# Kernel tuning notes

Hardware: AMD Instinct MI355X
Metric: run time of the kernel (lower is better)

Reference implementation:

```python
import jax, jax.numpy as jnp
import numpy as np

DIM = 256
D_STATE = 64
D_CONV = 4
EXPAND = 2
D_INNER = EXPAND * DIM          # 512
DT_RANK = DIM // 16             # 16, Mamba default dt_rank='auto'
LN_EPS = 1e-5


def setup_inputs() -> dict:
    key = jax.random.key(0)
    ks = jax.random.split(key, 8)
    B, L = 4, 1024
    s = lambda k, shape, fan: jax.random.normal(k, shape, jnp.float32) / np.sqrt(fan).astype(np.float32)
    inp = {}
    inp['x'] = jax.random.normal(ks[0], (B, L, DIM), jnp.float32)
    inp['C_SA'] = jax.random.normal(ks[1], (B, L, D_STATE), jnp.float32)
    # LayerNorm params
    inp['gamma'] = jnp.ones((DIM,), jnp.float32)
    inp['beta'] = jnp.zeros((DIM,), jnp.float32)
    # Mamba params
    inp['W_in'] = s(ks[2], (2 * D_INNER, DIM), DIM)
    inp['conv_w'] = s(ks[3], (D_INNER, 1, D_CONV), D_CONV)   # depthwise causal conv
    inp['conv_b'] = jnp.zeros((D_INNER,), jnp.float32)
    inp['W_x'] = s(ks[4], (DT_RANK + D_STATE, D_INNER), D_INNER)  # -> (dt_low_rank, B_ssm)
    inp['W_dt'] = s(ks[5], (D_INNER, DT_RANK), DT_RANK)
    # softplus-inverse of 0.01 so initial dt ~ 0.01 (Mamba dt init)
    inp['b_dt'] = jnp.log(jnp.expm1(jnp.full((D_INNER,), 0.01, jnp.float32)))
    # S4D-real init: A = -[1..N]
    inp['A_log'] = jnp.log(jnp.broadcast_to(jnp.arange(1, D_STATE + 1, dtype=jnp.float32), (D_INNER, D_STATE)))
    inp['D'] = jnp.ones((D_INNER,), jnp.float32)
    inp['W_out'] = s(ks[6], (DIM, D_INNER), D_INNER)
    return inp


def reference(x, C_SA, gamma, beta, W_in, conv_w, conv_b, W_x, W_dt, b_dt, A_log, D, W_out):
    B, L, _ = x.shape
    # --- LayerNorm ---
    mu = jnp.mean(x, axis=-1, keepdims=True)
    var = jnp.mean(jnp.square(x - mu), axis=-1, keepdims=True)
    xn = (x - mu) * jax.lax.rsqrt(var + LN_EPS) * gamma + beta
    # --- input projection and gate split ---
    xz = xn @ W_in.T                              # [B,L,2*Di]
    u, z = jnp.split(xz, 2, axis=-1)
    # --- causal depthwise conv1d + SiLU ---
    u_c = jax.lax.conv_general_dilated(
        u.transpose(0, 2, 1), conv_w, (1,), [(D_CONV - 1, 0)],
        feature_group_count=D_INNER,
        dimension_numbers=('NCH', 'OIH', 'NCH'))  # [B,Di,L]
    u = jax.nn.silu(u_c.transpose(0, 2, 1) + conv_b)  # [B,L,Di]
    # --- data-dependent SSM params (C comes from C_SA externally) ---
    dbl = u @ W_x.T                               # [B,L,dt_rank+N]
    dt = jax.nn.softplus(dbl[..., :DT_RANK] @ W_dt.T + b_dt)  # [B,L,Di]
    Bs = dbl[..., DT_RANK:]                       # [B,L,N]
    A = -jnp.exp(A_log)                           # [Di,N]
    # --- selective scan over time ---
    def step(h, t):
        dt_t, B_t, C_t, u_t = t                   # [B,Di],[B,N],[B,N],[B,Di]
        dA = jnp.exp(dt_t[..., None] * A)         # [B,Di,N]
        h = dA * h + (dt_t * u_t)[..., None] * B_t[:, None, :]
        y = jnp.einsum('bdn,bn->bd', h, C_t)
        return h, y
    h0 = jnp.zeros((B, D_INNER, D_STATE), x.dtype)
    xs = (dt.transpose(1, 0, 2), Bs.transpose(1, 0, 2),
          C_SA.transpose(1, 0, 2), u.transpose(1, 0, 2))
    _, ys = jax.lax.scan(step, h0, xs)            # ys: [L,B,Di]
    y = ys.transpose(1, 0, 2) + u * D             # skip connection
    y = y * jax.nn.silu(z)                        # gate
    return y @ W_out.T                            # [B,L,dim]
```

## Files before the change

kernel.cpp:

```cpp
#include <hip/hip_runtime.h>
#include <cstdint>
#include <cstddef>

#define B_    4
#define L_    1024
#define DIM_  256
#define DI_   512
#define NTOK  (B_*L_)
#define NC    32
#define CL    (L_/NC)

__device__ __forceinline__ float siluf_(float x){ return x / (1.0f + __expf(-x)); }
__device__ __forceinline__ float softplusf_(float x){
  return (x > 15.0f) ? x : log1pf(__expf(x));
}

__global__ __launch_bounds__(1024) void k_check(const float* __restrict__ A_log,
    int* __restrict__ flag){
  __shared__ int s_ok;
  int tid = threadIdx.x;
  if (tid == 0) s_ok = 1;
  __syncthreads();
  int ok = 1;
  for (int i = tid; i < 512 * 64; i += 1024){
    int n = i & 63;
    float ref = logf((float)(n + 1));
    float v = A_log[i];
    if (fabsf(v - ref) > 1e-5f * fmaxf(1.0f, fabsf(ref))) ok = 0;
  }
  if (!ok) atomicAnd(&s_ok, 0);
  __syncthreads();
  if (tid == 0) *flag = s_ok;
}

__global__ __launch_bounds__(256) void k_ln_stats(const float* __restrict__ x,
    float* __restrict__ stats){
  int tok  = blockIdx.x * 4 + (threadIdx.x >> 6);
  int lane = threadIdx.x & 63;
  float4 v = *(const float4*)(x + (size_t)tok * DIM_ + lane * 4);
  float s  = v.x + v.y + v.z + v.w;
  float sq = v.x*v.x + v.y*v.y + v.z*v.z + v.w*v.w;
  #pragma unroll
  for (int off = 32; off; off >>= 1){
    s  += __shfl_xor(s,  off, 64);
    sq += __shfl_xor(sq, off, 64);
  }
  if (lane == 0){
    float mu = s * (1.0f / DIM_);
    stats[tok*2]   = mu;
    stats[tok*2+1] = rsqrtf(sq * (1.0f / DIM_) - mu*mu + 1e-5f);
  }
}

__global__ __launch_bounds__(256) void k_gemm1(const float* __restrict__ x,
    const float* __restrict__ stats, const float* __restrict__ gamma,
    const float* __restrict__ beta, const float* __restrict__ Win,
    float* __restrict__ xz){
  __shared__ float As[16][64];
  __shared__ float Bs[16][64];
  int tid = threadIdx.x;
  int mBase = blockIdx.y * 64;
  int nBase = blockIdx.x * 64;
  int tx = tid & 15, ty = tid >> 4;
  int am = tid >> 2, ak = (tid & 3) << 2;
  float mu = stats[(mBase+am)*2], rs = stats[(mBase+am)*2+1];
  float acc[4][4] = {};
  for (int kt = 0; kt < 256; kt += 16){
    float4 av = *(const float4*)(x   + (size_t)(mBase+am)*256 + kt + ak);
    float4 bv = *(const float4*)(Win + (size_t)(nBase+am)*256 + kt + ak);
    float4 gv = *(const float4*)(gamma + kt + ak);
    float4 be = *(const float4*)(beta  + kt + ak);
    As[ak+0][am] = (av.x - mu) * rs * gv.x + be.x;
    As[ak+1][am] = (av.y - mu) * rs * gv.y + be.y;
    As[ak+2][am] = (av.z - mu) * rs * gv.z + be.z;
    As[ak+3][am] = (av.w - mu) * rs * gv.w + be.w;
    Bs[ak+0][am]=bv.x; Bs[ak+1][am]=bv.y; Bs[ak+2][am]=bv.z; Bs[ak+3][am]=bv.w;
    __syncthreads();
    #pragma unroll
    for (int kk = 0; kk < 16; kk++){
      float4 a = *(const float4*)&As[kk][ty*4];
      float4 b = *(const float4*)&Bs[kk][tx*4];
      float ar[4] = {a.x,a.y,a.z,a.w}, br[4] = {b.x,b.y,b.z,b.w};
      #pragma unroll
      for (int i=0;i<4;i++)
        #pragma unroll
        for (int j=0;j<4;j++)
          acc[i][j] += ar[i]*br[j];
    }
    __syncthreads();
  }
  #pragma unroll
  for (int i=0;i<4;i++){
    float4 o = make_float4(acc[i][0],acc[i][1],acc[i][2],acc[i][3]);
    *(float4*)(xz + (size_t)(mBase+ty*4+i)*1024 + nBase + tx*4) = o;
  }
}

__global__ __launch_bounds__(256) void k_conv(const float* __restrict__ xz,
    const float* __restrict__ cw, const float* __restrict__ cb,
    float* __restrict__ uc){
  int g = blockIdx.x * 256 + threadIdx.x;
  int d = g & 511;
  int tok = g >> 9;
  int t = tok & (L_ - 1);
  float w0 = cw[d*4+0], w1 = cw[d*4+1], w2 = cw[d*4+2], w3 = cw[d*4+3];
  const float* up = xz + (size_t)tok * 1024 + d;
  float acc = cb[d] + w3 * up[0];
  if (t >= 1) acc += w2 * up[-1 * 1024];
  if (t >= 2) acc += w1 * up[-2 * 1024];
  if (t >= 3) acc += w0 * up[-3 * 1024];
  uc[g] = siluf_(acc);
}

__global__ __launch_bounds__(320) void k_gemm2(const float* __restrict__ uc,
    const float* __restrict__ Wx, float* __restrict__ dbl){
  __shared__ float As[4 * 516];
  int tid = threadIdx.x;
  int mBase = blockIdx.x * 4;
  for (int idx = tid * 4; idx < 4 * 512; idx += 320 * 4){
    int r = idx >> 9, k = idx & 511;
    *(float4*)&As[r * 516 + k] = *(const float4*)(uc + (size_t)(mBase + r) * 512 + k);
  }
  __syncthreads();
  int n = tid >> 2;
  int r = tid & 3;
  const float* arow = &As[r * 516];
  const float* wp = Wx + (size_t)n * 512;
  float acc = 0.f;
  #pragma unroll 8
  for (int k4 = 0; k4 < 512; k4 += 4){
    float4 a = *(const float4*)&arow[k4];
    float4 w = *(const float4*)(wp + k4);
    acc += a.x*w.x + a.y*w.y + a.z*w.z + a.w*w.w;
  }
  dbl[(size_t)(mBase + r) * 80 + n] = acc;
}

__global__ __launch_bounds__(256) void k_dt(const float* __restrict__ dbl,
    const float* __restrict__ Wdt, const float* __restrict__ bdt,
    float* __restrict__ dt){
  int g = blockIdx.x * 256 + threadIdx.x;
  int d = g & 511; int m = g >> 9;
  float acc = bdt[d];
  const float* r = dbl + (size_t)m * 80;
  #pragma unroll
  for (int k = 0; k < 16; k++)
    acc += r[k] * Wdt[d * 16 + k];
  dt[g] = softplusf_(acc);
}

__global__ __launch_bounds__(256, 4) void k_scanA(const float* __restrict__ dt,
    const float* __restrict__ uc, const float* __restrict__ dbl,
    const float* __restrict__ A_log, const int* __restrict__ flagp,
    float* __restrict__ hseg, float* __restrict__ S){
  __shared__ float sB[CL][64];
  int tid  = threadIdx.x;
  int gw   = (blockIdx.x * 256 + tid) >> 6;
  int lane = tid & 63;
  int dsub = lane & 7, ngrp = lane >> 3;
  int grp = gw & 255;
  int c   = gw >> 8;
  int ch  = grp * 8 + dsub;
  int b = ch >> 9, d = ch & 511;
  int tbeg = c * CL;
  {
    const float* Bsrc = dbl + (size_t)b * L_ * 80 + (size_t)tbeg * 80 + 16;
    for (int i = tid; i < CL * 16; i += 256){
      int row = i >> 4, col = (i & 15) << 2;
      *(float4*)&sB[row][col] = *(const float4*)(Bsrc + row * 80 + col);
    }
  }
  __syncthreads();
  int fast = *flagp;
  const float* dtp = dt + (size_t)b * L_ * 512 + d;
  const float* ucp = uc + (size_t)b * L_ * 512 + d;
  float h[8] = {};
  float Ssum = 0.f;
  float st1 = (float)(ngrp * 8 + 1);
  float dtC[4], uC[4];
  #pragma unroll
  for (int j = 0; j < 4; j++){
    dtC[j] = dtp[(size_t)(tbeg+j) * 512];
    uC[j]  = ucp[(size_t)(tbeg+j) * 512];
  }
  if (fast){
    for (int t0 = tbeg; t0 < tbeg + CL; t0 += 4){
      float dtN[4], uN[4];
      if (t0 + 4 < tbeg + CL){
        #pragma unroll
        for (int j = 0; j < 4; j++){
          dtN[j] = dtp[(size_t)(t0+4+j) * 512];
          uN[j]  = ucp[(size_t)(t0+4+j) * 512];
        }
      }
      int tt = t0 - tbeg;
      #pragma unroll
      for (int j = 0; j < 4; j++){
        float4 b0 = *(const float4*)&sB[tt+j][ngrp*8];
        float4 b1 = *(const float4*)&sB[tt+j][ngrp*8+4];
        float sc = dtC[j] * uC[j];
        Ssum += dtC[j];
        float e1 = __expf(-dtC[j]);
        float e2 = e1 * e1;
        float e4 = e2 * e2;
        float dA0 = __expf(-dtC[j] * st1);
        float dA1 = dA0 * e1;
        float dA2 = dA0 * e2;
        float dA3 = dA1 * e2;
        h[0] = dA0 * h[0] + sc * b0.x;
        h[1] = dA1 * h[1] + sc * b0.y;
        h[2] = dA2 * h[2] + sc * b0.z;
        h[3] = dA3 * h[3] + sc * b0.w;
        dA0 *= e4; dA1 *= e4; dA2 *= e4; dA3 *= e4;
        h[4] = dA0 * h[4] + sc * b1.x;
        h[5] = dA1 * h[5] + sc * b1.y;
        h[6] = dA2 * h[6] + sc * b1.z;
        h[7] = dA3 * h[7] + sc * b1.w;
      }
      #pragma unroll
      for (int j = 0; j < 4; j++){ dtC[j] = dtN[j]; uC[j] = uN[j]; }
    }
  } else {
    float Aa[8];
    float4 a0 = *(const float4*)(A_log + (size_t)d*64 + ngrp*8);
    float4 a1 = *(const float4*)(A_log + (size_t)d*64 + ngrp*8 + 4);
    Aa[0]=-__expf(a0.x); Aa[1]=-__expf(a0.y); Aa[2]=-__expf(a0.z); Aa[3]=-__expf(a0.w);
    Aa[4]=-__expf(a1.x); Aa[5]=-__expf(a1.y); Aa[6]=-__expf(a1.z); Aa[7]=-__expf(a1.w);
    for (int t0 = tbeg; t0 < tbeg + CL; t0 += 4){
      float dtN[4], uN[4];
      if (t0 + 4 < tbeg + CL){
        #pragma unroll
        for (int j = 0; j < 4; j++){
          dtN[j] = dtp[(size_t)(t0+4+j) * 512];
          uN[j]  = ucp[(size_t)(t0+4+j) * 512];
        }
      }
      int tt = t0 - tbeg;
      #pragma unroll
      for (int j = 0; j < 4; j++){
        float4 b0 = *(const float4*)&sB[tt+j][ngrp*8];
        float4 b1 = *(const float4*)&sB[tt+j][ngrp*8+4];
        float Bv[8] = {b0.x,b0.y,b0.z,b0.w,b1.x,b1.y,b1.z,b1.w};
        float sc = dtC[j] * uC[j];
        Ssum += dtC[j];
        #pragma unroll
        for (int i = 0; i < 8; i++)
          h[i] = __expf(dtC[j] * Aa[i]) * h[i] + sc * Bv[i];
      }
      #pragma unroll
      for (int j = 0; j < 4; j++){ dtC[j] = dtN[j]; uC[j] = uN[j]; }
    }
  }
  float* hp = hseg + ((size_t)(c * 2048 + ch)) * 64 + ngrp*8;
  *(float4*)hp     = make_float4(h[0],h[1],h[2],h[3]);
  *(float4*)(hp+4) = make_float4(h[4],h[5],h[6],h[7]);
  if (ngrp == 0) S[c * 2048 + ch] = Ssum;
}

__global__ __launch_bounds__(256) void k_scanB(float* __restrict__ hseg,
    const float* __restrict__ S, const float* __restrict__ A_log,
    const int* __restrict__ flagp){
  int ch   = (blockIdx.x * 256 + threadIdx.x) >> 6;
  int lane = threadIdx.x & 63;
  int d = ch & 511;
  int fast = *flagp;
  float A = fast ? -(float)(lane + 1) : -__expf(A_log[(size_t)d * 64 + lane]);
  float hc = 0.f;
  #pragma unroll 8
  for (int c = 0; c < NC; c++){
    size_t idx = ((size_t)(c * 2048 + ch)) * 64 + lane;
    float hf = hseg[idx];
    hseg[idx] = hc;
    float Sv = S[c * 2048 + ch];
    hc = hf + __expf(A * Sv) * hc;
  }
}

__global__ __launch_bounds__(256, 4) void k_scanC(const float* __restrict__ dt,
    const float* __restrict__ uc, const float* __restrict__ dbl,
    const float* __restrict__ C_SA, const float* __restrict__ A_log,
    const int* __restrict__ flagp,
    const float* __restrict__ hin, const float* __restrict__ xz,
    const float* __restrict__ Dp, float* __restrict__ ys){
  __shared__ float sB[CL][64];
  __shared__ float sC[CL][64];
  __shared__ float sZ[CL][32];
  int tid  = threadIdx.x;
  int gw   = (blockIdx.x * 256 + tid) >> 6;
  int lane = tid & 63;
  int dsub = lane & 7, ngrp = lane >> 3;
  int grp = gw & 255;
  int c   = gw >> 8;
  int ch  = grp * 8 + dsub;
  int b = ch >> 9, d = ch & 511;
  int tbeg = c * CL;
  int ch0 = ((blockIdx.x * 4) & 255) * 8;
  int d0  = ch0 & 511;
  {
    const float* Bsrc = dbl  + (size_t)b * L_ * 80 + (size_t)tbeg * 80 + 16;
    const float* Csrc = C_SA + (size_t)b * L_ * 64 + (size_t)tbeg * 64;
    for (int i = tid; i < CL * 16; i += 256){
      int row = i >> 4, col = (i & 15) << 2;
      *(float4*)&sB[row][col] = *(const float4*)(Bsrc + row * 80 + col);
      *(float4*)&sC[row][col] = *(const float4*)(Csrc + row * 64 + col);
    }
    const float* Zsrc = xz + (size_t)b * L_ * 1024 + (size_t)tbeg * 1024 + 512 + d0;
    int zr = tid >> 3, zc = (tid & 7) << 2;
    *(float4*)&sZ[zr][zc] = *(const float4*)(Zsrc + zr * 1024 + zc);
  }
  __syncthreads();
  int fast = *flagp;
  const float* dtp = dt + (size_t)b * L_ * 512 + d;
  const float* ucp = uc + (size_t)b * L_ * 512 + d;
  float Dv = Dp[d];
  int zcol = (grp & 3) * 8 + dsub;
  float*       yw  = ys + (size_t)b * L_ * 512 + d;
  float h[8];
  {
    const float* hp = hin + ((size_t)(c * 2048 + ch)) * 64 + ngrp*8;
    float4 h0 = *(const float4*)hp;
    float4 h1 = *(const float4*)(hp + 4);
    h[0]=h0.x; h[1]=h0.y; h[2]=h0.z; h[3]=h0.w;
    h[4]=h1.x; h[5]=h1.y; h[6]=h1.z; h[7]=h1.w;
  }
  float st1 = (float)(ngrp * 8 + 1);
  float dtC[4], uC[4];
  #pragma unroll
  for (int j = 0; j < 4; j++){
    dtC[j] = dtp[(size_t)(tbeg+j) * 512];
    uC[j]  = ucp[(size_t)(tbeg+j) * 512];
  }
  if (fast){
    for (int t0 = tbeg; t0 < tbeg + CL; t0 += 4){
      float dtN[4], uN[4];
      if (t0 + 4 < tbeg + CL){
        #pragma unroll
        for (int j = 0; j < 4; j++){
          dtN[j] = dtp[(size_t)(t0+4+j) * 512];
          uN[j]  = ucp[(size_t)(t0+4+j) * 512];
        }
      }
      int tt = t0 - tbeg;
      float yp[4];
      #pragma unroll
      for (int j = 0; j < 4; j++){
        float4 b0 = *(const float4*)&sB[tt+j][ngrp*8];
        float4 b1 = *(const float4*)&sB[tt+j][ngrp*8+4];
        float4 c0 = *(const float4*)&sC[tt+j][ngrp*8];
        float4 c1 = *(const float4*)&sC[tt+j][ngrp*8+4];
        float sc = dtC[j] * uC[j];
        float e1 = __expf(-dtC[j]);
        float e2 = e1 * e1;
        float e4 = e2 * e2;
        float dA0 = __expf(-dtC[j] * st1);
        float dA1 = dA0 * e1;
        float dA2 = dA0 * e2;
        float dA3 = dA1 * e2;
        h[0] = dA0 * h[0] + sc * b0.x;
        h[1] = dA1 * h[1] + sc * b0.y;
        h[2] = dA2 * h[2] + sc * b0.z;
        h[3] = dA3 * h[3] + sc * b0.w;
        float y0 = h[0] * c0.x;
        float y1 = h[1] * c0.y;
        float y2 = h[2] * c0.z;
        float y3 = h[3] * c0.w;
        dA0 *= e4; dA1 *= e4; dA2 *= e4; dA3 *= e4;
        h[4] = dA0 * h[4] + sc * b1.x;
        h[5] = dA1 * h[5] + sc * b1.y;
        h[6] = dA2 * h[6] + sc * b1.z;
        h[7] = dA3 * h[7] + sc * b1.w;
        y0 += h[4] * c1.x;
        y1 += h[5] * c1.y;
        y2 += h[6] * c1.z;
        y3 += h[7] * c1.w;
        yp[j] = (y0 + y1) + (y2 + y3);
      }
      #pragma unroll
      for (int off = 8; off < 64; off <<= 1){
        #pragma unroll
        for (int j = 0; j < 4; j++)
          yp[j] += __shfl_xor(yp[j], off, 64);
      }
      if (ngrp == 0){
        #pragma unroll
        for (int j = 0; j < 4; j++){
          float z = sZ[tt+j][zcol];
          yw[(size_t)(t0+j) * 512] = (yp[j] + uC[j] * Dv) * siluf_(z);
        }
      }
      #pragma unroll
      for (int j = 0; j < 4; j++){ dtC[j] = dtN[j]; uC[j] = uN[j]; }
    }
  } else {
    float Aa[8];
    float4 a0 = *(const float4*)(A_log + (size_t)d*64 + ngrp*8);
    float4 a1 = *(const float4*)(A_log + (size_t)d*64 + ngrp*8 + 4);
    Aa[0]=-__expf(a0.x); Aa[1]=-__expf(a0.y); Aa[2]=-__expf(a0.z); Aa[3]=-__expf(a0.w);
    Aa[4]=-__expf(a1.x); Aa[5]=-__expf(a1.y); Aa[6]=-__expf(a1.z); Aa[7]=-__expf(a1.w);
    for (int t0 = tbeg; t0 < tbeg + CL; t0 += 4){
      float dtN[4], uN[4];
      if (t0 + 4 < tbeg + CL){
        #pragma unroll
        for (int j = 0; j < 4; j++){
          dtN[j] = dtp[(size_t)(t0+4+j) * 512];
          uN[j]  = ucp[(size_t)(t0+4+j) * 512];
        }
      }
      int tt = t0 - tbeg;
      float yp[4];
      #pragma unroll
      for (int j = 0; j < 4; j++){
        float4 b0 = *(const float4*)&sB[tt+j][ngrp*8];
        float4 b1 = *(const float4*)&sB[tt+j][ngrp*8+4];
        float4 c0 = *(const float4*)&sC[tt+j][ngrp*8];
        float4 c1 = *(const float4*)&sC[tt+j][ngrp*8+4];
        float sc = dtC[j] * uC[j];
        h[0] = __expf(dtC[j] * Aa[0]) * h[0] + sc * b0.x;
        h[1] = __expf(dtC[j] * Aa[1]) * h[1] + sc * b0.y;
        h[2] = __expf(dtC[j] * Aa[2]) * h[2] + sc * b0.z;
        h[3] = __expf(dtC[j] * Aa[3]) * h[3] + sc * b0.w;
        float y0 = h[0] * c0.x;
        float y1 = h[1] * c0.y;
        float y2 = h[2] * c0.z;
        float y3 = h[3] * c0.w;
        h[4] = __expf(dtC[j] * Aa[4]) * h[4] + sc * b1.x;
        h[5] = __expf(dtC[j] * Aa[5]) * h[5] + sc * b1.y;
        h[6] = __expf(dtC[j] * Aa[6]) * h[6] + sc * b1.z;
        h[7] = __expf(dtC[j] * Aa[7]) * h[7] + sc * b1.w;
        y0 += h[4] * c1.x;
        y1 += h[5] * c1.y;
        y2 += h[6] * c1.z;
        y3 += h[7] * c1.w;
        yp[j] = (y0 + y1) + (y2 + y3);
      }
      #pragma unroll
      for (int off = 8; off < 64; off <<= 1){
        #pragma unroll
        for (int j = 0; j < 4; j++)
          yp[j] += __shfl_xor(yp[j], off, 64);
      }
      if (ngrp == 0){
        #pragma unroll
        for (int j = 0; j < 4; j++){
          float z = sZ[tt+j][zcol];
          yw[(size_t)(t0+j) * 512] = (yp[j] + uC[j] * Dv) * siluf_(z);
        }
      }
      #pragma unroll
      for (int j = 0; j < 4; j++){ dtC[j] = dtN[j]; uC[j] = uN[j]; }
    }
  }
}

__global__ __launch_bounds__(256) void k_gemm3(const float* __restrict__ Ag,
    const float* __restrict__ Wout, float* __restrict__ out){
  __shared__ float As[32 * 34];
  __shared__ float Bs[32 * 34];
  int tid = threadIdx.x;
  int nBase = blockIdx.x * 32;
  int mBase = blockIdx.y * 32;
  int tx = tid & 15, ty = tid >> 4;
  int ar = tid >> 3;
  int ak = (tid & 7) << 2;
  float acc[2][2] = {};
  for (int kt = 0; kt < 512; kt += 32){
    float4 av = *(const float4*)(Ag   + (size_t)(mBase+ar)*512 + kt + ak);
    float4 bv = *(const float4*)(Wout + (size_t)(nBase+ar)*512 + kt + ak);
    As[(ak+0)*34 + ar] = av.x; As[(ak+1)*34 + ar] = av.y;
    As[(ak+2)*34 + ar] = av.z; As[(ak+3)*34 + ar] = av.w;
    Bs[(ak+0)*34 + ar] = bv.x; Bs[(ak+1)*34 + ar] = bv.y;
    Bs[(ak+2)*34 + ar] = bv.z; Bs[(ak+3)*34 + ar] = bv.w;
    __syncthreads();
    #pragma unroll
    for (int kk = 0; kk < 32; kk++){
      float2 a = *(const float2*)&As[kk*34 + ty*2];
      float2 b = *(const float2*)&Bs[kk*34 + tx*2];
      acc[0][0] += a.x*b.x; acc[0][1] += a.x*b.y;
      acc[1][0] += a.y*b.x; acc[1][1] += a.y*b.y;
    }
    __syncthreads();
  }
  #pragma unroll
  for (int i = 0; i < 2; i++){
    float2 o = make_float2(acc[i][0], acc[i][1]);
    *(float2*)(out + (size_t)(mBase+ty*2+i)*256 + nBase + tx*2) = o;
  }
}

extern "C" void kernel_launch(void* const* d_in, const int* in_sizes, int n_in,
                              void* d_out, int out_size, void* d_ws, size_t ws_size,
                              hipStream_t stream) {
  const float* x      = (const float*)d_in[0];
  const float* C_SA   = (const float*)d_in[1];
  const float* gamma  = (const float*)d_in[2];
  const float* beta   = (const float*)d_in[3];
  const float* W_in   = (const float*)d_in[4];
  const float* conv_w = (const float*)d_in[5];
  const float* conv_b = (const float*)d_in[6];
  const float* W_x    = (const float*)d_in[7];
  const float* W_dt   = (const float*)d_in[8];
  const float* b_dt   = (const float*)d_in[9];
  const float* A_log  = (const float*)d_in[10];
  const float* Dw     = (const float*)d_in[11];
  const float* W_out  = (const float*)d_in[12];
  float* out = (float*)d_out;

  float* ws    = (float*)d_ws;
  float* stats = ws;
  int*   flag  = (int*)(ws + 8192);
  float* xz    = ws    + 16384;
  float* uc    = xz    + 4194304;
  float* dbl   = uc    + 2097152;
  float* dtb   = dbl   + 327680;
  float* hseg  = dtb   + 2097152;
  float* S     = hseg  + 4194304;
  float* ysb   = S     + 65536;

  k_check<<<1, 1024, 0, stream>>>(A_log, flag);
  k_ln_stats<<<NTOK/4, 256, 0, stream>>>(x, stats);
  k_gemm1<<<dim3(16, 64), 256, 0, stream>>>(x, stats, gamma, beta, W_in, xz);
  k_conv <<<(NTOK*512)/256, 256, 0, stream>>>(xz, conv_w, conv_b, uc);
  k_gemm2<<<1024, 320, 0, stream>>>(uc, W_x, dbl);
  k_dt   <<<(NTOK*512)/256, 256, 0, stream>>>(dbl, W_dt, b_dt, dtb);
  k_scanA<<<NC*64, 256, 0, stream>>>(dtb, uc, dbl, A_log, flag, hseg, S);
  k_scanB<<<512, 256, 0, stream>>>(hseg, S, A_log, flag);
  k_scanC<<<NC*64, 256, 0, stream>>>(dtb, uc, dbl, C_SA, A_log, flag, hseg, xz, Dw, ysb);
  k_gemm3<<<dim3(8, 128), 256, 0, stream>>>(ysb, W_out, out);
}
```

Before: 258.6 us.

## Use 64x64 register-tiled split-K output GEMM with separate reduction kernel

```diff
diff --git a/kernel.cpp b/kernel.cpp
--- a/kernel.cpp
+++ b/kernel.cpp
@@ -452,39 +452,54 @@
   }
 }
 
-__global__ __launch_bounds__(256) void k_gemm3(const float* __restrict__ Ag,
-    const float* __restrict__ Wout, float* __restrict__ out){
-  __shared__ float As[32 * 34];
-  __shared__ float Bs[32 * 34];
+__global__ __launch_bounds__(256) void k_gemm3s(const float* __restrict__ Ag,
+    const float* __restrict__ Wout, float* __restrict__ pbuf){
+  __shared__ float As[16][64];
+  __shared__ float Bs[16][64];
   int tid = threadIdx.x;
-  int nBase = blockIdx.x * 32;
-  int mBase = blockIdx.y * 32;
+  int nBase = blockIdx.x * 64;
+  int mBase = blockIdx.y * 64;
+  int kBase = blockIdx.z * 128;
   int tx = tid & 15, ty = tid >> 4;
-  int ar = tid >> 3;
-  int ak = (tid & 7) << 2;
-  float acc[2][2] = {};
-  for (int kt = 0; kt < 512; kt += 32){
-    float4 av = *(const float4*)(Ag   + (size_t)(mBase+ar)*512 + kt + ak);
-    float4 bv = *(const float4*)(Wout + (size_t)(nBase+ar)*512 + kt + ak);
-    As[(ak+0)*34 + ar] = av.x; As[(ak+1)*34 + ar] = av.y;
-    As[(ak+2)*34 + ar] = av.z; As[(ak+3)*34 + ar] = av.w;
-    Bs[(ak+0)*34 + ar] = bv.x; Bs[(ak+1)*34 + ar] = bv.y;
-    Bs[(ak+2)*34 + ar] = bv.z; Bs[(ak+3)*34 + ar] = bv.w;
+  int am = tid >> 2, ak = (tid & 3) << 2;
+  float acc[4][4] = {};
+  for (int kt = kBase; kt < kBase + 128; kt += 16){
+    float4 av = *(const float4*)(Ag   + (size_t)(mBase+am)*512 + kt + ak);
+    float4 bv = *(const float4*)(Wout + (size_t)(nBase+am)*512 + kt + ak);
+    As[ak+0][am]=av.x; As[ak+1][am]=av.y; As[ak+2][am]=av.z; As[ak+3][am]=av.w;
+    Bs[ak+0][am]=bv.x; Bs[ak+1][am]=bv.y; Bs[ak+2][am]=bv.z; Bs[ak+3][am]=bv.w;
     __syncthreads();
     #pragma unroll
-    for (int kk = 0; kk < 32; kk++){
-      float2 a = *(const float2*)&As[kk*34 + ty*2];
-      float2 b = *(const float2*)&Bs[kk*34 + tx*2];
-      acc[0][0] += a.x*b.x; acc[0][1] += a.x*b.y;
-      acc[1][0] += a.y*b.x; acc[1][1] += a.y*b.y;
+    for (int kk = 0; kk < 16; kk++){
+      float4 a = *(const float4*)&As[kk][ty*4];
+      float4 b = *(const float4*)&Bs[kk][tx*4];
+      float ar[4] = {a.x,a.y,a.z,a.w}, br[4] = {b.x,b.y,b.z,b.w};
+      #pragma unroll
+      for (int i=0;i<4;i++)
+        #pragma unroll
+        for (int j=0;j<4;j++)
+          acc[i][j] += ar[i]*br[j];
     }
     __syncthreads();
   }
+  float* pw = pbuf + (size_t)blockIdx.z * (NTOK * 256);
   #pragma unroll
-  for (int i = 0; i < 2; i++){
-    float2 o = make_float2(acc[i][0], acc[i][1]);
-    *(float2*)(out + (size_t)(mBase+ty*2+i)*256 + nBase + tx*2) = o;
-  }
+  for (int i=0;i<4;i++){
+    float4 o = make_float4(acc[i][0],acc[i][1],acc[i][2],acc[i][3]);
+    *(float4*)(pw + (size_t)(mBase+ty*4+i)*256 + nBase + tx*4) = o;
+  }
+}
+
+__global__ __launch_bounds__(256) void k_g3red(const float* __restrict__ pbuf,
+    float* __restrict__ out){
+  int i4 = (blockIdx.x * 256 + threadIdx.x) * 4;
+  float4 a = *(const float4*)(pbuf + i4);
+  float4 b = *(const float4*)(pbuf + (size_t)NTOK*256   + i4);
+  float4 c = *(const float4*)(pbuf + (size_t)NTOK*512   + i4);
+  float4 d = *(const float4*)(pbuf + (size_t)NTOK*768   + i4);
+  float4 o = make_float4((a.x+b.x)+(c.x+d.x), (a.y+b.y)+(c.y+d.y),
+                         (a.z+b.z)+(c.z+d.z), (a.w+b.w)+(c.w+d.w));
+  *(float4*)(out + i4) = o;
 }
 
 extern "C" void kernel_launch(void* const* d_in, const int* in_sizes, int n_in,
@@ -515,6 +530,7 @@
   float* hseg  = dtb   + 2097152;
   float* S     = hseg  + 4194304;
   float* ysb   = S     + 65536;
+  float* pbuf  = hseg;
 
   k_check<<<1, 1024, 0, stream>>>(A_log, flag);
   k_ln_stats<<<NTOK/4, 256, 0, stream>>>(x, stats);
@@ -525,5 +541,6 @@
   k_scanA<<<NC*64, 256, 0, stream>>>(dtb, uc, dbl, A_log, flag, hseg, S);
   k_scanB<<<512, 256, 0, stream>>>(hseg, S, A_log, flag);
   k_scanC<<<NC*64, 256, 0, stream>>>(dtb, uc, dbl, C_SA, A_log, flag, hseg, xz, Dw, ysb);
-  k_gemm3<<<dim3(8, 128), 256, 0, stream>>>(ysb, W_out, out);
-}
+  k_gemm3s<<<dim3(4, 64, 4), 256, 0, stream>>>(ysb, W_out, pbuf);
+  k_g3red<<<NTOK*256/1024, 256, 0, stream>>>(pbuf, out);
+}
```

New measurement: 248.8 us. 1.04x faster.
